# Kernel tuning notes

Hardware: AMD Instinct MI355X
Metric: run time of the kernel (lower is better)

## Reference

```python
import jax, jax.numpy as jnp
import numpy as np

B, D, S = 16384, 2048, 512      # batch, input_dim, sideinfo_dim
E, H1, H2 = 8, 1024, 512        # subexpert_num, subexpert_unit
EPS = 1e-5                       # BatchNorm eps (torch default)


def setup_inputs() -> dict:
    key = jax.random.key(0)
    ks = jax.random.split(key, 16)
    inp = {
        "input": jax.random.normal(ks[0], (B, D), jnp.float32),
        "sideinfo": jax.random.normal(ks[1], (B, S), jnp.float32),
        # expert layer 1: Linear(D->H1) per expert, batched over E
        "W1": jax.random.normal(ks[2], (E, D, H1), jnp.float32) / np.sqrt(D),
        "b1": jax.random.normal(ks[3], (E, H1), jnp.float32) * 0.01,
        "gamma1": 1.0 + 0.01 * jax.random.normal(ks[4], (E, H1), jnp.float32),
        "beta1": jax.random.normal(ks[5], (E, H1), jnp.float32) * 0.01,
        "mean1": jax.random.normal(ks[6], (E, H1), jnp.float32) * 0.01,
        "var1": jax.random.uniform(ks[7], (E, H1), jnp.float32, 0.5, 1.5),
        # expert layer 2: Linear(H1->H2) per expert
        "W2": jax.random.normal(ks[8], (E, H1, H2), jnp.float32) / np.sqrt(H1),
        "b2": jax.random.normal(ks[9], (E, H2), jnp.float32) * 0.01,
        "gamma2": 1.0 + 0.01 * jax.random.normal(ks[10], (E, H2), jnp.float32),
        "beta2": jax.random.normal(ks[11], (E, H2), jnp.float32) * 0.01,
        "mean2": jax.random.normal(ks[12], (E, H2), jnp.float32) * 0.01,
        "var2": jax.random.uniform(ks[13], (E, H2), jnp.float32, 0.5, 1.5),
        # gate: Linear(S->E) + softmax
        "Wg": jax.random.normal(ks[14], (S, E), jnp.float32) / np.sqrt(S),
        "bg": jax.random.normal(ks[15], (E,), jnp.float32) * 0.01,
    }
    return inp


def _bn(x, gamma, beta, mean, var):
    # eval-mode BatchNorm1d with per-expert running stats; x: [B,E,H]
    return (x - mean) * (gamma * jax.lax.rsqrt(var + EPS)) + beta


def reference(input, sideinfo, W1, b1, gamma1, beta1, mean1, var1,
              W2, b2, gamma2, beta2, mean2, var2, Wg, bg):
    # all E expert MLPs as two batched GEMMs (dropout is identity in eval)
    h = jnp.einsum('bd,edh->beh', input, W1) + b1            # [B,E,H1]
    h = jax.nn.relu(_bn(h, gamma1, beta1, mean1, var1))
    o = jnp.einsum('beh,eho->beo', h, W2) + b2               # [B,E,H2]
    o = jax.nn.relu(_bn(o, gamma2, beta2, mean2, var2))
    gate = jax.nn.softmax(sideinfo @ Wg + bg, axis=1)        # [B,E]
    return jnp.einsum('beo,be->bo', o, gate)                 # [B,H2]
```

## Files before the change

### kernel.cpp

```cpp
#include <hip/hip_runtime.h>
#include <hip/hip_bf16.h>

static constexpr int B_  = 16384;
static constexpr int D_  = 2048;
static constexpr int S_  = 512;
static constexpr int E_  = 8;
static constexpr int H1_ = 1024;
static constexpr int H2_ = 512;
static constexpr float EPS_ = 1e-5f;

typedef __bf16 bf16x8 __attribute__((ext_vector_type(8)));
typedef float  f32x4  __attribute__((ext_vector_type(4)));

static __device__ __forceinline__ unsigned short f2bf(float f) {
    unsigned u = __float_as_uint(f);
    unsigned r = (u + 0x7fffu + ((u >> 16) & 1u)) >> 16;
    return (unsigned short)r;
}


__global__ void cvt_bf16_kernel(const float* __restrict__ in, ushort* __restrict__ out, long n) {
    long i = ((long)blockIdx.x * blockDim.x + threadIdx.x) * 4;
    long stride = (long)gridDim.x * blockDim.x * 4;
    for (; i < n; i += stride) {
        float4 v = *(const float4*)(in + i);
        ushort4 o;
        o.x = f2bf(v.x); o.y = f2bf(v.y); o.z = f2bf(v.z); o.w = f2bf(v.w);
        *(ushort4*)(out + i) = o;
    }
}

__global__ void transpose_cvt_kernel(const float* __restrict__ in, ushort* __restrict__ out,
                                     int R, int C) {
    __shared__ float t[64][65];
    int nbr = R >> 6, nbc = C >> 6;
    int bid = blockIdx.x;
    int e = bid / (nbr * nbc);
    int rem = bid % (nbr * nbc);
    int br = (rem / nbc) << 6, bc = (rem % nbc) << 6;
    const float* ip = in + (size_t)e * R * C;
    ushort* op = out + (size_t)e * R * C;
    int tcol = (threadIdx.x & 15) * 4;
    int trow = threadIdx.x >> 4;
#pragma unroll
    for (int p = 0; p < 4; p++) {
        int r = trow + p * 16;
        float4 v = *(const float4*)(ip + (size_t)(br + r) * C + bc + tcol);
        t[r][tcol + 0] = v.x; t[r][tcol + 1] = v.y; t[r][tcol + 2] = v.z; t[r][tcol + 3] = v.w;
    }
    __syncthreads();
#pragma unroll
    for (int p = 0; p < 4; p++) {
        int c = trow + p * 16;
        ushort4 o;
        o.x = f2bf(t[tcol + 0][c]);
        o.y = f2bf(t[tcol + 1][c]);
        o.z = f2bf(t[tcol + 2][c]);
        o.w = f2bf(t[tcol + 3][c]);
        *(ushort4*)(op + (size_t)(bc + c) * R + br + tcol) = o;
    }
}

__global__ void fold_bn_kernel(const float* __restrict__ gamma, const float* __restrict__ beta,
                               const float* __restrict__ mean, const float* __restrict__ var,
                               const float* __restrict__ bias,
                               float* __restrict__ Sv, float* __restrict__ Tv, int n) {
    int i = blockIdx.x * 256 + threadIdx.x;
    if (i < n) {
        float s = gamma[i] * rsqrtf(var[i] + EPS_);
        Sv[i] = s;
        Tv[i] = (bias[i] - mean[i]) * s + beta[i];
    }
}

__global__ void gate_kernel(const float* __restrict__ side, const float* __restrict__ Wg,
                            const float* __restrict__ bg, float* __restrict__ gate) {
    int wid = threadIdx.x >> 6, lane = threadIdx.x & 63;
    int b = blockIdx.x * 4 + wid;
    const float* sp = side + (size_t)b * S_ + lane * 8;
    float4 v0 = *(const float4*)sp;
    float4 v1 = *(const float4*)(sp + 4);
    float sv[8] = {v0.x, v0.y, v0.z, v0.w, v1.x, v1.y, v1.z, v1.w};
    float acc[E_] = {0,0,0,0,0,0,0,0};
    const float* wrow = Wg + (size_t)(lane * 8) * E_;
#pragma unroll
    for (int j = 0; j < 8; j++) {
        float4 w0 = *(const float4*)(wrow + j * E_);
        float4 w1 = *(const float4*)(wrow + j * E_ + 4);
        acc[0] += sv[j] * w0.x; acc[1] += sv[j] * w0.y;
        acc[2] += sv[j] * w0.z; acc[3] += sv[j] * w0.w;
        acc[4] += sv[j] * w1.x; acc[5] += sv[j] * w1.y;
        acc[6] += sv[j] * w1.z; acc[7] += sv[j] * w1.w;
    }
#pragma unroll
    for (int off = 32; off; off >>= 1)
#pragma unroll
        for (int e = 0; e < E_; e++) acc[e] += __shfl_xor(acc[e], off, 64);
    float m = -1e30f;
#pragma unroll
    for (int e = 0; e < E_; e++) { acc[e] += bg[e]; m = fmaxf(m, acc[e]); }
    float s = 0.f;
#pragma unroll
    for (int e = 0; e < E_; e++) { acc[e] = __expf(acc[e] - m); s += acc[e]; }
    float inv = 1.f / s;
    if (lane < E_) gate[(size_t)b * E_ + lane] = acc[lane] * inv;
}


__device__ __forceinline__ void g2lds16(const void* g, void* l) {
    __builtin_amdgcn_global_load_lds((const __attribute__((address_space(1))) unsigned int*)g,
                                     (__attribute__((address_space(3))) unsigned int*)l,
                                     16, 0, 0);
}

#define BAR()      asm volatile("s_barrier" ::: "memory")
#define WAITVM(n)  asm volatile("s_waitcnt vmcnt(" #n ")" ::: "memory")
#define MFMA(a,b,c) __builtin_amdgcn_mfma_f32_16x16x32_bf16((a),(b),(c),0,0,0)


template<int EPI>
__global__ __launch_bounds__(512, 2)
void gemm8(const ushort* __restrict__ A, const ushort* __restrict__ Bt, long aBatch,
           const float* __restrict__ Sv, const float* __restrict__ Tv,
           ushort* __restrict__ hout, float* __restrict__ outp, const float* __restrict__ gate,
           int M, int N, int K, int tilesN, int tilesM)
{
    extern __shared__ char smem[];

    const int NT  = K >> 6;
    const int tpe = tilesM * tilesN;

    const int nwg = gridDim.x, per = nwg >> 3;
    const int b0  = blockIdx.x;
    const int bid = (b0 & 7) * per + (b0 >> 3);

    const int e   = bid / tpe;
    const int rem = bid % tpe;
    const int tm  = rem / tilesN, tn = rem % tilesN;

    const char* aBase = (const char*)(A + (size_t)e * aBatch + (size_t)tm * 256 * K);
    const char* bBase = (const char*)(Bt + (size_t)e * N * K + (size_t)tn * 256 * K);
    const size_t rowB = (size_t)K * 2;
    const size_t half2 = 64 * rowB;
    const size_t half1 = 128 * rowB;

    const int tid = threadIdx.x, w = tid >> 6, lane = tid & 63;
    const int wm = w >> 2, wn = w & 3;

    const int srow = tid >> 3;
    const int scol_sw = ((tid & 7) * 16) ^ ((srow & 7) << 4);
    const int ldsW = w * 1024;

    const int lr = lane & 15;
    const int cks0 = ((lane >> 4) * 16) ^ ((lane & 7) << 4);
    const int cks1 = (64 + (lane >> 4) * 16) ^ ((lane & 7) << 4);
    const char* rdA0 = smem + 65536 + (wm * 128 + lr) * 128 + cks0;
    const char* rdA1 = smem + 65536 + (wm * 128 + lr) * 128 + cks1;
    const char* rdB0 = smem + (wn * 64 + lr) * 128 + cks0;
    const char* rdB1 = smem + (wn * 64 + lr) * 128 + cks1;

#define STG(gp, ldsoff) do { \
        g2lds16((gp), smem + (ldsoff)); \
        g2lds16((gp) + half2, smem + (ldsoff) + 8192); } while (0)

    const char* ga = aBase + (size_t)srow * rowB + scol_sw;
    const char* gb = bBase + (size_t)srow * rowB + scol_sw;

    f32x4 acc[8][4] = {};
    bf16x8 a0[8], a1[8], bb0[4], bb1[4];

    STG(ga,               65536 + 0     + 0     + ldsW);
    STG(ga + half1,       65536 + 0     + 16384 + ldsW);
    STG(gb,               0     + 0     + 0     + ldsW);
    STG(gb + half1,       0     + 0     + 16384 + ldsW);
    STG(ga + 128,         65536 + 32768 + 0     + ldsW);
    STG(ga + half1 + 128, 65536 + 32768 + 16384 + ldsW);
    STG(gb + 128,         0     + 32768 + 0     + ldsW);
    WAITVM(6);
    BAR();

    const char* sp3 = gb + half1 + 128;
    const char* sp0 = ga + 256;
    const char* sp1 = ga + half1 + 256;
    const char* sp2 = gb + 256;

#pragma unroll 2
    for (int t = 0; t < NT; ++t) {
        const int bi  = t & 1;
        const int oAr = bi * 32768;
        const int oAs = 65536 + bi * 32768;
        const int oB  = bi * 32768;
        const int oBx = (bi ^ 1) * 32768;

#pragma unroll
        for (int mf = 0; mf < 8; ++mf) a0[mf] = *(const bf16x8*)(rdA0 + oAr + mf * 2048);
#pragma unroll
        for (int nf = 0; nf < 4; ++nf) bb0[nf] = *(const bf16x8*)(rdB0 + oB + nf * 2048);
        if (t < NT - 1) STG(sp3, oBx + 16384 + ldsW);
        BAR();
        __builtin_amdgcn_s_setprio(1);
#pragma unroll
        for (int mf = 0; mf < 8; ++mf) {
            acc[mf][0] = MFMA(a0[mf], bb0[0], acc[mf][0]);
            acc[mf][1] = MFMA(a0[mf], bb0[1], acc[mf][1]);
        }
        __builtin_amdgcn_s_setprio(0);
        BAR();
#pragma unroll
        for (int mf = 0; mf < 8; ++mf) a1[mf] = *(const bf16x8*)(rdA1 + oAr + mf * 2048);
        if (t < NT - 2) STG(sp0, oAs + 0 + ldsW);
        BAR();
        __builtin_amdgcn_s_setprio(1);
#pragma unroll
        for (int mf = 0; mf < 8; ++mf) {
            acc[mf][2] = MFMA(a0[mf], bb0[2], acc[mf][2]);
            acc[mf][3] = MFMA(a0[mf], bb0[3], acc[mf][3]);
        }
        __builtin_amdgcn_s_setprio(0);
        BAR();
#pragma unroll
        for (int nf = 0; nf < 4; ++nf) bb1[nf] = *(const bf16x8*)(rdB1 + oB + nf * 2048);
        if (t < NT - 2) STG(sp1, oAs + 16384 + ldsW);
        BAR();
        __builtin_amdgcn_s_setprio(1);
#pragma unroll
        for (int mf = 0; mf < 8; ++mf) {
            acc[mf][0] = MFMA(a1[mf], bb1[0], acc[mf][0]);
            acc[mf][1] = MFMA(a1[mf], bb1[1], acc[mf][1]);
        }
        __builtin_amdgcn_s_setprio(0);
        BAR();
        if (t < NT - 2) STG(sp2, oB + 0 + ldsW);
        BAR();
        __builtin_amdgcn_s_setprio(1);
#pragma unroll
        for (int mf = 0; mf < 8; ++mf) {
            acc[mf][2] = MFMA(a1[mf], bb1[2], acc[mf][2]);
            acc[mf][3] = MFMA(a1[mf], bb1[3], acc[mf][3]);
        }
        __builtin_amdgcn_s_setprio(0);
        if (t < NT - 2)       { WAITVM(6); }
        else if (t == NT - 2) { WAITVM(0); }
        BAR();

        sp3 += 128; sp0 += 128; sp1 += 128; sp2 += 128;
    }

    const int rbase = tm * 256 + wm * 128 + (lane >> 4) * 4;
    const int cbase = tn * 256 + wn * 64 + lr;
    if (EPI == 1) {
#pragma unroll
        for (int nf = 0; nf < 4; ++nf) {
            const int col = cbase + nf * 16;
            const float s = Sv[e * N + col];
            const float tt = Tv[e * N + col];
#pragma unroll
            for (int mf = 0; mf < 8; ++mf) {
                const int row0 = rbase + mf * 16;
                f32x4 v = acc[mf][nf];
#pragma unroll
                for (int r = 0; r < 4; ++r) {
                    float x = v[r] * s + tt;
                    x = x > 0.f ? x : 0.f;
                    hout[((size_t)e * M + row0 + r) * N + col] = f2bf(x);
                }
            }
        }
    }
#undef STG
}


__global__ __launch_bounds__(512, 2)
void gemm2e(const ushort* __restrict__ H, const ushort* __restrict__ W2T,
            const float* __restrict__ Sv, const float* __restrict__ Tv,
            const float* __restrict__ gate, float* __restrict__ outp)
{
    extern __shared__ char smem[];

    const int b0 = blockIdx.x;
    const int bid = (b0 & 7) * 32 + (b0 >> 3);
    const int tm = bid >> 1, tn = bid & 1;

    const size_t rowB  = (size_t)H1_ * 2;
    const size_t strAE = (size_t)B_ * H1_ * 2;
    const size_t strBE = (size_t)H2_ * H1_ * 2;
    const size_t half2 = 64 * rowB;
    const size_t halfB = 128 * rowB;

    const int tid = threadIdx.x, w = tid >> 6, lane = tid & 63;
    const int wm = w >> 2, wn = w & 3;

    const int srow = tid >> 3;
    const int scol_sw = ((tid & 7) * 16) ^ ((srow & 7) << 4);
    const int ldsW = w * 1024;

    const int lr = lane & 15;
    const int cks0 = ((lane >> 4) * 16) ^ ((lane & 7) << 4);
    const int cks1 = (64 + (lane >> 4) * 16) ^ ((lane & 7) << 4);
    const char* rdA0 = smem + 65536 + (wm * 64 + lr) * 128 + cks0;
    const char* rdA1 = smem + 65536 + (wm * 64 + lr) * 128 + cks1;
    const char* rdB0 = smem + (wn * 64 + lr) * 128 + cks0;
    const char* rdB1 = smem + (wn * 64 + lr) * 128 + cks1;

    const char* ga = (const char*)H + (size_t)tm * 128 * rowB + (size_t)srow * rowB + scol_sw;
    const char* gb = (const char*)W2T + (size_t)tn * 256 * rowB + (size_t)srow * rowB + scol_sw;

#define STG2(gp, ldsoff) do { \
        g2lds16((gp), smem + (ldsoff)); \
        g2lds16((gp) + half2, smem + (ldsoff) + 8192); } while (0)

    f32x4 acc[4][4] = {};
    f32x4 oacc[4][4] = {};
    bf16x8 a0[4], a1[4], bb0[4], bb1[4];

    g2lds16(ga,               smem + 65536 + 0     + 0    + ldsW);
    g2lds16(ga + half2,       smem + 65536 + 0     + 8192 + ldsW);
    STG2(gb,                  0     + 0     + ldsW);
    STG2(gb + halfB,          0     + 16384 + ldsW);
    g2lds16(ga + 128,         smem + 65536 + 16384 + 0    + ldsW);
    g2lds16(ga + half2 + 128, smem + 65536 + 16384 + 8192 + ldsW);
    STG2(gb + 128,            32768 + 0     + ldsW);
    WAITVM(4);
    BAR();

    const int rbase = tm * 128 + wm * 64 + (lane >> 4) * 4;
    const int cbase = tn * 256 + wn * 64 + lr;

    for (int t = 0; t < 128; ++t) {
        const int bi  = t & 1;
        const int oA  = bi * 16384;
        const int oB  = bi * 32768;

        const int t1 = t + 1, t2 = t + 2;
        const char* gB1 = gb + (size_t)(t1 >> 4) * strBE + (t1 & 15) * 128;
        const char* gA2 = ga + (size_t)(t2 >> 4) * strAE + (t2 & 15) * 128;
        const char* gB2 = gb + (size_t)(t2 >> 4) * strBE + (t2 & 15) * 128;
        const int oA2 = 65536 + ((t2 & 1) * 16384);
        const int oB1x = (t1 & 1) * 32768;
        const int oB2 = (t2 & 1) * 32768;

#pragma unroll
        for (int mf = 0; mf < 4; ++mf) a0[mf] = *(const bf16x8*)(rdA0 + oA + mf * 2048);
#pragma unroll
        for (int nf = 0; nf < 4; ++nf) bb0[nf] = *(const bf16x8*)(rdB0 + oB + nf * 2048);
        if (t1 < 128) STG2(gB1 + halfB, oB1x + 16384 + ldsW);
        BAR();
        __builtin_amdgcn_s_setprio(1);
#pragma unroll
        for (int mf = 0; mf < 4; ++mf) {
            acc[mf][0] = MFMA(a0[mf], bb0[0], acc[mf][0]);
            acc[mf][1] = MFMA(a0[mf], bb0[1], acc[mf][1]);
        }
        __builtin_amdgcn_s_setprio(0);
        BAR();
#pragma unroll
        for (int mf = 0; mf < 4; ++mf) a1[mf] = *(const bf16x8*)(rdA1 + oA + mf * 2048);
        if (t2 < 128) {
            g2lds16(gA2, smem + oA2 + 0 + ldsW);
        }
        BAR();
        __builtin_amdgcn_s_setprio(1);
#pragma unroll
        for (int mf = 0; mf < 4; ++mf) {
            acc[mf][2] = MFMA(a0[mf], bb0[2], acc[mf][2]);
            acc[mf][3] = MFMA(a0[mf], bb0[3], acc[mf][3]);
        }
        __builtin_amdgcn_s_setprio(0);
        BAR();
#pragma unroll
        for (int nf = 0; nf < 4; ++nf) bb1[nf] = *(const bf16x8*)(rdB1 + oB + nf * 2048);
        if (t2 < 128) {
            g2lds16(gA2 + half2, smem + oA2 + 8192 + ldsW);
        }
        BAR();
        __builtin_amdgcn_s_setprio(1);
#pragma unroll
        for (int mf = 0; mf < 4; ++mf) {
            acc[mf][0] = MFMA(a1[mf], bb1[0], acc[mf][0]);
            acc[mf][1] = MFMA(a1[mf], bb1[1], acc[mf][1]);
        }
        __builtin_amdgcn_s_setprio(0);
        BAR();
        if (t2 < 128) STG2(gB2, oB2 + 0 + ldsW);
        BAR();
        __builtin_amdgcn_s_setprio(1);
#pragma unroll
        for (int mf = 0; mf < 4; ++mf) {
            acc[mf][2] = MFMA(a1[mf], bb1[2], acc[mf][2]);
            acc[mf][3] = MFMA(a1[mf], bb1[3], acc[mf][3]);
        }
        __builtin_amdgcn_s_setprio(0);
        if (t < 126)       { WAITVM(4); }
        else if (t == 126) { WAITVM(0); }
        BAR();

        if ((t & 15) == 15) {
            const int e = t >> 4;
            float sc[4], tc[4];
#pragma unroll
            for (int nf = 0; nf < 4; ++nf) {
                sc[nf] = Sv[e * H2_ + cbase + nf * 16];
                tc[nf] = Tv[e * H2_ + cbase + nf * 16];
            }
#pragma unroll
            for (int mf = 0; mf < 4; ++mf) {
#pragma unroll
                for (int r = 0; r < 4; ++r) {
                    const int row = rbase + mf * 16 + r;
                    const float g = gate[(size_t)row * E_ + e];
#pragma unroll
                    for (int nf = 0; nf < 4; ++nf) {
                        float x = acc[mf][nf][r] * sc[nf] + tc[nf];
                        x = x > 0.f ? x : 0.f;
                        oacc[mf][nf][r] += g * x;
                    }
                }
            }
#pragma unroll
            for (int mf = 0; mf < 4; ++mf)
#pragma unroll
                for (int nf = 0; nf < 4; ++nf)
                    acc[mf][nf] = (f32x4){0.f, 0.f, 0.f, 0.f};
        }
    }

#pragma unroll
    for (int mf = 0; mf < 4; ++mf) {
#pragma unroll
        for (int r = 0; r < 4; ++r) {
            const int row = rbase + mf * 16 + r;
#pragma unroll
            for (int nf = 0; nf < 4; ++nf)
                outp[(size_t)row * H2_ + cbase + nf * 16] = oacc[mf][nf][r];
        }
    }
#undef STG2
}


extern "C" void kernel_launch(void* const* d_in, const int* in_sizes, int n_in,
                              void* d_out, int out_size, void* d_ws, size_t ws_size,
                              hipStream_t stream) {
    (void)in_sizes; (void)n_in; (void)out_size; (void)ws_size;

    const float* input    = (const float*)d_in[0];
    const float* sideinfo = (const float*)d_in[1];
    const float* W1   = (const float*)d_in[2];
    const float* b1   = (const float*)d_in[3];
    const float* g1   = (const float*)d_in[4];
    const float* be1  = (const float*)d_in[5];
    const float* m1   = (const float*)d_in[6];
    const float* v1   = (const float*)d_in[7];
    const float* W2   = (const float*)d_in[8];
    const float* b2   = (const float*)d_in[9];
    const float* g2   = (const float*)d_in[10];
    const float* be2  = (const float*)d_in[11];
    const float* m2   = (const float*)d_in[12];
    const float* v2   = (const float*)d_in[13];
    const float* Wg   = (const float*)d_in[14];
    const float* bg   = (const float*)d_in[15];

    char* w = (char*)d_ws;
    size_t off = 0;
    auto carve = [&](size_t bytes) {
        void* p = w + off;
        off += (bytes + 255) & ~(size_t)255;
        return p;
    };
    ushort* Abf  = (ushort*)carve((size_t)B_ * D_ * 2);
    ushort* W1T  = (ushort*)carve((size_t)E_ * H1_ * D_ * 2);
    ushort* W2T  = (ushort*)carve((size_t)E_ * H2_ * H1_ * 2);
    ushort* hbuf = (ushort*)carve((size_t)E_ * B_ * H1_ * 2);
    float*  S1   = (float*)carve((size_t)E_ * H1_ * 4);
    float*  T1   = (float*)carve((size_t)E_ * H1_ * 4);
    float*  S2   = (float*)carve((size_t)E_ * H2_ * 4);
    float*  T2   = (float*)carve((size_t)E_ * H2_ * 4);
    float*  gatep = (float*)carve((size_t)B_ * E_ * 4);

    float* outp = (float*)d_out;

    hipFuncSetAttribute(reinterpret_cast<const void*>(&gemm8<1>),
                        hipFuncAttributeMaxDynamicSharedMemorySize, 131072);
    hipFuncSetAttribute(reinterpret_cast<const void*>(&gemm2e),
                        hipFuncAttributeMaxDynamicSharedMemorySize, 98304);

    cvt_bf16_kernel<<<4096, 256, 0, stream>>>(input, Abf, (long)B_ * D_);
    transpose_cvt_kernel<<<E_ * (D_ / 64) * (H1_ / 64), 256, 0, stream>>>(W1, W1T, D_, H1_);
    transpose_cvt_kernel<<<E_ * (H1_ / 64) * (H2_ / 64), 256, 0, stream>>>(W2, W2T, H1_, H2_);
    fold_bn_kernel<<<(E_ * H1_ + 255) / 256, 256, 0, stream>>>(g1, be1, m1, v1, b1, S1, T1, E_ * H1_);
    fold_bn_kernel<<<(E_ * H2_ + 255) / 256, 256, 0, stream>>>(g2, be2, m2, v2, b2, S2, T2, E_ * H2_);
    gate_kernel<<<B_ / 4, 256, 0, stream>>>(sideinfo, Wg, bg, gatep);

    gemm8<1><<<E_ * (B_ / 256) * (H1_ / 256), 512, 131072, stream>>>(
        Abf, W1T, 0L, S1, T1, hbuf, nullptr, nullptr, B_, H1_, D_, H1_ / 256, B_ / 256);

    gemm2e<<<(B_ / 128) * (H2_ / 256), 512, 98304, stream>>>(
        hbuf, W2T, S2, T2, gatep, outp);
}
```

Before: 739.7 us.

## Restructure GEMM main loop to one barrier per K-tile with register-prefetched fragments

Replaces the multi-phase ping-pong main loop, which had about eight barriers per K-tile, with a simpler double-buffered loop. Global-to-LDS copies of the next tile are issued up front, and A/B fragments are prefetched into registers in halves so LDS reads overlap the MFMA blocks. The only barrier is at the end of each tile, after a full vmcnt drain. This is meant to cut barrier and synchronisation overhead. The cost is a shallower global prefetch depth, one tile ahead with a full wait, which may expose memory latency.

```diff
diff --git a/kernel.cpp b/kernel.cpp
--- a/kernel.cpp
+++ b/kernel.cpp
@@ -167,83 +167,90 @@
     const char* gb = bBase + (size_t)srow * rowB + scol_sw;
 
     f32x4 acc[8][4] = {};
-    bf16x8 a0[8], a1[8], bb0[4], bb1[4];
-
-    STG(ga,               65536 + 0     + 0     + ldsW);
-    STG(ga + half1,       65536 + 0     + 16384 + ldsW);
-    STG(gb,               0     + 0     + 0     + ldsW);
-    STG(gb + half1,       0     + 0     + 16384 + ldsW);
-    STG(ga + 128,         65536 + 32768 + 0     + ldsW);
-    STG(ga + half1 + 128, 65536 + 32768 + 16384 + ldsW);
-    STG(gb + 128,         0     + 32768 + 0     + ldsW);
-    WAITVM(6);
+    bf16x8 aC[4], aN[4], bC[4], bN[4];
+
+    STG(ga,         65536 + 0 + 0     + ldsW);
+    STG(ga + half1, 65536 + 0 + 16384 + ldsW);
+    STG(gb,         0     + 0 + 0     + ldsW);
+    STG(gb + half1, 0     + 0 + 16384 + ldsW);
+    WAITVM(0);
     BAR();
 
-    const char* sp3 = gb + half1 + 128;
-    const char* sp0 = ga + 256;
-    const char* sp1 = ga + half1 + 256;
-    const char* sp2 = gb + 256;
+#pragma unroll
+    for (int mf = 0; mf < 4; ++mf) aC[mf] = *(const bf16x8*)(rdA0 + mf * 2048);
+#pragma unroll
+    for (int nf = 0; nf < 4; ++nf) bC[nf] = *(const bf16x8*)(rdB0 + nf * 2048);
+
+    const char* spA0 = ga + 128;
+    const char* spA1 = ga + half1 + 128;
+    const char* spB0 = gb + 128;
+    const char* spB1 = gb + half1 + 128;
 
 #pragma unroll 2
     for (int t = 0; t < NT; ++t) {
-        const int bi  = t & 1;
-        const int oAr = bi * 32768;
-        const int oAs = 65536 + bi * 32768;
-        const int oB  = bi * 32768;
-        const int oBx = (bi ^ 1) * 32768;
-
-#pragma unroll
-        for (int mf = 0; mf < 8; ++mf) a0[mf] = *(const bf16x8*)(rdA0 + oAr + mf * 2048);
-#pragma unroll
-        for (int nf = 0; nf < 4; ++nf) bb0[nf] = *(const bf16x8*)(rdB0 + oB + nf * 2048);
-        if (t < NT - 1) STG(sp3, oBx + 16384 + ldsW);
-        BAR();
-        __builtin_amdgcn_s_setprio(1);
-#pragma unroll
-        for (int mf = 0; mf < 8; ++mf) {
-            acc[mf][0] = MFMA(a0[mf], bb0[0], acc[mf][0]);
-            acc[mf][1] = MFMA(a0[mf], bb0[1], acc[mf][1]);
-        }
-        __builtin_amdgcn_s_setprio(0);
-        BAR();
-#pragma unroll
-        for (int mf = 0; mf < 8; ++mf) a1[mf] = *(const bf16x8*)(rdA1 + oAr + mf * 2048);
-        if (t < NT - 2) STG(sp0, oAs + 0 + ldsW);
-        BAR();
-        __builtin_amdgcn_s_setprio(1);
-#pragma unroll
-        for (int mf = 0; mf < 8; ++mf) {
-            acc[mf][2] = MFMA(a0[mf], bb0[2], acc[mf][2]);
-            acc[mf][3] = MFMA(a0[mf], bb0[3], acc[mf][3]);
-        }
-        __builtin_amdgcn_s_setprio(0);
-        BAR();
-#pragma unroll
-        for (int nf = 0; nf < 4; ++nf) bb1[nf] = *(const bf16x8*)(rdB1 + oB + nf * 2048);
-        if (t < NT - 2) STG(sp1, oAs + 16384 + ldsW);
-        BAR();
-        __builtin_amdgcn_s_setprio(1);
-#pragma unroll
-        for (int mf = 0; mf < 8; ++mf) {
-            acc[mf][0] = MFMA(a1[mf], bb1[0], acc[mf][0]);
-            acc[mf][1] = MFMA(a1[mf], bb1[1], acc[mf][1]);
-        }
-        __builtin_amdgcn_s_setprio(0);
-        BAR();
-        if (t < NT - 2) STG(sp2, oB + 0 + ldsW);
-        BAR();
-        __builtin_amdgcn_s_setprio(1);
-#pragma unroll
-        for (int mf = 0; mf < 8; ++mf) {
-            acc[mf][2] = MFMA(a1[mf], bb1[2], acc[mf][2]);
-            acc[mf][3] = MFMA(a1[mf], bb1[3], acc[mf][3]);
-        }
-        __builtin_amdgcn_s_setprio(0);
-        if (t < NT - 2)       { WAITVM(6); }
-        else if (t == NT - 2) { WAITVM(0); }
-        BAR();
-
-        sp3 += 128; sp0 += 128; sp1 += 128; sp2 += 128;
+        const int bi   = t & 1;
+        const int oR   = bi * 32768;
+        const int oRN  = (bi ^ 1) * 32768;
+        const int oSA  = 65536 + (bi ^ 1) * 32768;
+        const int oSB  = (bi ^ 1) * 32768;
+        const bool more = (t < NT - 1);
+
+#pragma unroll
+        for (int mf = 0; mf < 4; ++mf) aN[mf] = *(const bf16x8*)(rdA0 + oR + (4 + mf) * 2048);
+        if (more) {
+            STG(spA0, oSA + 0 + ldsW);
+            STG(spA1, oSA + 16384 + ldsW);
+        }
+        __builtin_amdgcn_s_setprio(1);
+#pragma unroll
+        for (int mf = 0; mf < 4; ++mf)
+#pragma unroll
+            for (int nf = 0; nf < 4; ++nf)
+                acc[mf][nf] = MFMA(aC[mf], bC[nf], acc[mf][nf]);
+        __builtin_amdgcn_s_setprio(0);
+
+#pragma unroll
+        for (int mf = 0; mf < 4; ++mf) aC[mf] = *(const bf16x8*)(rdA1 + oR + mf * 2048);
+#pragma unroll
+        for (int nf = 0; nf < 4; ++nf) bN[nf] = *(const bf16x8*)(rdB1 + oR + nf * 2048);
+        if (more) STG(spB0, oSB + 0 + ldsW);
+        __builtin_amdgcn_s_setprio(1);
+#pragma unroll
+        for (int mf = 0; mf < 4; ++mf)
+#pragma unroll
+            for (int nf = 0; nf < 4; ++nf)
+                acc[4 + mf][nf] = MFMA(aN[mf], bC[nf], acc[4 + mf][nf]);
+        __builtin_amdgcn_s_setprio(0);
+
+#pragma unroll
+        for (int mf = 0; mf < 4; ++mf) aN[mf] = *(const bf16x8*)(rdA1 + oR + (4 + mf) * 2048);
+        if (more) STG(spB1, oSB + 16384 + ldsW);
+        __builtin_amdgcn_s_setprio(1);
+#pragma unroll
+        for (int mf = 0; mf < 4; ++mf)
+#pragma unroll
+            for (int nf = 0; nf < 4; ++nf)
+                acc[mf][nf] = MFMA(aC[mf], bN[nf], acc[mf][nf]);
+        __builtin_amdgcn_s_setprio(0);
+
+        __builtin_amdgcn_s_setprio(1);
+#pragma unroll
+        for (int mf = 0; mf < 4; ++mf)
+#pragma unroll
+            for (int nf = 0; nf < 4; ++nf)
+                acc[4 + mf][nf] = MFMA(aN[mf], bN[nf], acc[4 + mf][nf]);
+        __builtin_amdgcn_s_setprio(0);
+
+        if (more) {
+            WAITVM(0);
+            BAR();
+#pragma unroll
+            for (int mf = 0; mf < 4; ++mf) aC[mf] = *(const bf16x8*)(rdA0 + oRN + mf * 2048);
+#pragma unroll
+            for (int nf = 0; nf < 4; ++nf) bC[nf] = *(const bf16x8*)(rdB0 + oRN + nf * 2048);
+        }
+
+        spA0 += 128; spA1 += 128; spB0 += 128; spB1 += 128;
     }
 
     const int rbase = tm * 256 + wm * 128 + (lane >> 4) * 4;
```

Result: no change. 745.4 us (+0.8%).
